# Performance work log

Measured on AMD Instinct MI355X. Metric: run time of the kernel, lower is better.

The kernel has to match this reference:

```python
import jax, jax.numpy as jnp
import numpy as np

DIM = 64
LEN = 256


def setup_inputs() -> dict:
    key = jax.random.key(0)
    ks = jax.random.split(key, 9)
    b, h, B = 4, 8, 16
    q = jax.random.normal(ks[0], (b, h, B, LEN, DIM), dtype=jnp.float32)
    k = jax.random.normal(ks[1], (b, h, B, LEN, DIM), dtype=jnp.float32)
    s = 1.0 / np.sqrt(DIM)
    Wq = jax.random.normal(ks[2], (1, DIM), dtype=jnp.float32) * s
    bq = jnp.ones((1,), dtype=jnp.float32)
    Wk = jax.random.normal(ks[3], (1, DIM), dtype=jnp.float32) * s
    bk = jnp.ones((1,), dtype=jnp.float32)
    sl = 1.0 / np.sqrt(LEN)
    W1 = jax.random.normal(ks[4], (1, LEN), dtype=jnp.float32) * sl
    W2a = jax.random.normal(ks[5], (LEN, LEN), dtype=jnp.float32) * sl
    W2b = jax.random.normal(ks[6], (1, LEN), dtype=jnp.float32) * sl
    return {"q": q, "k": k, "Wq": Wq, "bq": bq, "Wk": Wk, "bk": bk,
            "W1": W1, "W2a": W2a, "W2b": W2b}


def reference(q, k, Wq, bq, Wk, bk, W1, W2a, W2b):
    # Sigma_q/k: [b,h,B,L,1]
    Sigma_q = jnp.einsum('bhgid,od->bhgio', q, Wq) + bq
    Sigma_k = jnp.einsum('bhgjd,od->bhgjo', k, Wk) + bk
    # similarity: [b,h,B,L,L]
    sim = jnp.einsum('bhgid,bhgjd->bhgij', q, k)
    # outer product of the scalar projections: [b,h,B,L,L]
    Sigma = Sigma_q * jnp.swapaxes(Sigma_k, -1, -2)
    # zero the diagonal (sim - diag_embed(diag(sim)))
    eye = jnp.eye(sim.shape[-1], dtype=sim.dtype)
    sim_norm = sim * (1.0 - eye)
    # mlp1: Linear(L,1) over last axis -> [b,h,B,L]
    theta = jnp.einsum('bhgij,j->bhgi', sim_norm, W1[0])
    # mlp2: Linear(L,L) -> LeakyReLU(0.1) -> Linear(L,1) over axis i -> [b,h,B,1]
    hdn = jnp.einsum('bhgi,oi->bhgo', theta, W2a)
    hdn = jnp.where(hdn >= 0, hdn, 0.1 * hdn)
    theta = jnp.einsum('bhgi,oi->bhgo', hdn, W2b)[..., None]  # [b,h,B,1,1]
    sim = sim * Sigma
    attn = jax.nn.softmax(sim, axis=-1) * (sim > theta)
    return attn
```

## Files before the change

kernel.cpp:

```cpp
#include <hip/hip_runtime.h>
#include <math.h>

#define LL 256
#define DD 64

__launch_bounds__(512, 2)
__global__ void fused_attn_kernel(const float* __restrict__ q,
                                  const float* __restrict__ k,
                                  const float* __restrict__ Wq,
                                  const float* __restrict__ bq,
                                  const float* __restrict__ Wk,
                                  const float* __restrict__ bk,
                                  const float* __restrict__ W1,
                                  const float* __restrict__ W2a,
                                  const float* __restrict__ W2b,
                                  float* __restrict__ out)
{
    extern __shared__ float sm[];
    float* qT   = sm;
    float* kT   = sm + 64 * 256;
    float* sPq  = sm + 2 * 64 * 256;
    float* sPk  = sPq + 256;
    float* sPqk = sPk + 256;
    float* sTh  = sPqk + 256;
    float* sSq  = sTh + 256;
    float* sSk  = sSq + 256;
    float* kwred= sSk + 256;
    float* kw_s = kwred + 512;
    float* sRed = kw_s + 64;

    const int tid  = threadIdx.x;
    const int lane = tid & 63;
    const int wid  = tid >> 6;
    const int g    = blockIdx.x;
    const size_t gbase = (size_t)g * (LL * DD);
    const float4* q4 = (const float4*)(q + gbase);
    const float4* k4 = (const float4*)(k + gbase);

    const int dc = tid & 15;
    const float4 wq4 = ((const float4*)Wq)[dc];
    const float4 wk4 = ((const float4*)Wk)[dc];

    float kw0 = 0.f, kw1 = 0.f, kw2 = 0.f, kw3 = 0.f;

#pragma unroll
    for (int it = 0; it < 8; ++it) {
        const int f = it * 512 + tid;
        const int j = f >> 4;
        const float4 vq = q4[f];
        const float4 vk = k4[f];
        const int db = dc * 4;
        const int p  = db & 28;
        const int jx = j ^ p;
        qT[(db + 0) * 256 + jx] = vq.x;  kT[(db + 0) * 256 + jx] = vk.x;
        qT[(db + 1) * 256 + jx] = vq.y;  kT[(db + 1) * 256 + jx] = vk.y;
        qT[(db + 2) * 256 + jx] = vq.z;  kT[(db + 2) * 256 + jx] = vk.z;
        qT[(db + 3) * 256 + jx] = vq.w;  kT[(db + 3) * 256 + jx] = vk.w;

        const float w1j = W1[j];
        kw0 += w1j * vk.x; kw1 += w1j * vk.y; kw2 += w1j * vk.z; kw3 += w1j * vk.w;

        float pq  = vq.x * wq4.x + vq.y * wq4.y + vq.z * wq4.z + vq.w * wq4.w;
        float pk  = vk.x * wk4.x + vk.y * wk4.y + vk.z * wk4.z + vk.w * wk4.w;
        float pqk = vq.x * vk.x + vq.y * vk.y + vq.z * vk.z + vq.w * vk.w;
#pragma unroll
        for (int m = 1; m < 16; m <<= 1) {
            pq  += __shfl_xor(pq,  m);
            pk  += __shfl_xor(pk,  m);
            pqk += __shfl_xor(pqk, m);
        }
        if (dc == 0) { sPq[j] = pq; sPk[j] = pk; sPqk[j] = pqk; }
    }
    kw0 += __shfl_xor(kw0, 16); kw0 += __shfl_xor(kw0, 32);
    kw1 += __shfl_xor(kw1, 16); kw1 += __shfl_xor(kw1, 32);
    kw2 += __shfl_xor(kw2, 16); kw2 += __shfl_xor(kw2, 32);
    kw3 += __shfl_xor(kw3, 16); kw3 += __shfl_xor(kw3, 32);
    if (lane < 16) {
        float4 kv; kv.x = kw0; kv.y = kw1; kv.z = kw2; kv.w = kw3;
        ((float4*)kwred)[wid * 16 + lane] = kv;
    }
    __syncthreads();

    if (tid < 64) {
        float s = 0.f;
#pragma unroll
        for (int w = 0; w < 8; ++w) s += kwred[w * 64 + tid];
        kw_s[tid] = s;
    }
    __syncthreads();

    const float bq0 = bq[0], bk0 = bk[0];
    if (tid < 256) {
        const int i = tid;
        float qkw = 0.f;
#pragma unroll
        for (int d = 0; d < 64; ++d)
            qkw += qT[d * 256 + (i ^ (d & 28))] * kw_s[d];
        sTh[i] = qkw - W1[i] * sPqk[i];
        sSq[i] = sPq[i] + bq0;
        sSk[i] = sPk[i] + bk0;
    }
    __syncthreads();

    {
        const int o = tid >> 1, ih = tid & 1;
        const float4* wrow = (const float4*)W2a + o * 64 + ih * 32;
        const float4* th4  = (const float4*)sTh + ih * 32;
        float h = 0.f;
#pragma unroll 8
        for (int c = 0; c < 32; ++c) {
            const float4 wv = wrow[c];
            const float4 tv = th4[c];
            h += wv.x * tv.x + wv.y * tv.y + wv.z * tv.z + wv.w * tv.w;
        }
        h += __shfl_xor(h, 1);
        float contrib = 0.f;
        if (ih == 0) {
            const float hl = (h >= 0.f) ? h : 0.1f * h;
            contrib = hl * W2b[o];
        }
#pragma unroll
        for (int m = 1; m < 64; m <<= 1) contrib += __shfl_xor(contrib, m);
        if (lane == 0) sRed[wid] = contrib;
    }
    __syncthreads();

    const int rg = tid >> 4;
    const int cg = tid & 15;
    const int i0 = rg * 8;

    float acc[8][16];
#pragma unroll
    for (int r = 0; r < 8; ++r)
#pragma unroll
        for (int c = 0; c < 16; ++c) acc[r][c] = 0.f;

#pragma unroll 4
    for (int kk = 0; kk < 64; ++kk) {
        const float* qr = qT + kk * 256;
        const float* kr = kT + kk * 256;
        const int p = kk & 28;
        const float4 qa = *(const float4*)(qr + ((i0    ) ^ p));
        const float4 qb = *(const float4*)(qr + ((i0 + 4) ^ p));
        float4 kf[4];
        kf[0] = *(const float4*)(kr + ((cg * 4      ) ^ p));
        kf[1] = *(const float4*)(kr + ((cg * 4 +  64) ^ p));
        kf[2] = *(const float4*)(kr + ((cg * 4 + 128) ^ p));
        kf[3] = *(const float4*)(kr + ((cg * 4 + 192) ^ p));
        const float qv[8] = {qa.x, qa.y, qa.z, qa.w, qb.x, qb.y, qb.z, qb.w};
#pragma unroll
        for (int r = 0; r < 8; ++r) {
#pragma unroll
            for (int m = 0; m < 4; ++m) {
                acc[r][m * 4 + 0] += qv[r] * kf[m].x;
                acc[r][m * 4 + 1] += qv[r] * kf[m].y;
                acc[r][m * 4 + 2] += qv[r] * kf[m].z;
                acc[r][m * 4 + 3] += qv[r] * kf[m].w;
            }
        }
    }

    const float th_sc = sRed[0] + sRed[1] + sRed[2] + sRed[3] +
                        sRed[4] + sRed[5] + sRed[6] + sRed[7];
    float sq[8];
#pragma unroll
    for (int r = 0; r < 8; ++r) sq[r] = sSq[i0 + r];
    float sk[16];
#pragma unroll
    for (int m = 0; m < 4; ++m)
#pragma unroll
        for (int e = 0; e < 4; ++e) sk[m * 4 + e] = sSk[m * 64 + cg * 4 + e];

    float* og = out + (size_t)g * (LL * LL);

#pragma unroll
    for (int r = 0; r < 8; ++r) {
        float mx = -INFINITY;
#pragma unroll
        for (int c = 0; c < 16; ++c) {
            const float lg = acc[r][c] * sq[r] * sk[c];
            mx = fmaxf(mx, lg);
        }
        mx = fmaxf(mx, __shfl_xor(mx, 1));
        mx = fmaxf(mx, __shfl_xor(mx, 2));
        mx = fmaxf(mx, __shfl_xor(mx, 4));
        mx = fmaxf(mx, __shfl_xor(mx, 8));
        float sum = 0.f;
#pragma unroll
        for (int c = 0; c < 16; ++c) {
            const float lg = acc[r][c] * sq[r] * sk[c];
            const float pe = __expf(lg - mx);
            sum += pe;
            acc[r][c] = (lg > th_sc) ? pe : 0.f;
        }
        sum += __shfl_xor(sum, 1);
        sum += __shfl_xor(sum, 2);
        sum += __shfl_xor(sum, 4);
        sum += __shfl_xor(sum, 8);
        const float rinv = 1.0f / sum;
        const int row_off = (i0 + r) * 256 + cg * 4;
#pragma unroll
        for (int m = 0; m < 4; ++m) {
            float4 v;
            v.x = acc[r][m * 4 + 0] * rinv;
            v.y = acc[r][m * 4 + 1] * rinv;
            v.z = acc[r][m * 4 + 2] * rinv;
            v.w = acc[r][m * 4 + 3] * rinv;
            *(float4*)(og + row_off + m * 64) = v;
        }
    }
}

extern "C" void kernel_launch(void* const* d_in, const int* in_sizes, int n_in,
                              void* d_out, int out_size, void* d_ws, size_t ws_size,
                              hipStream_t stream) {
    const float* q   = (const float*)d_in[0];
    const float* k   = (const float*)d_in[1];
    const float* Wq  = (const float*)d_in[2];
    const float* bq  = (const float*)d_in[3];
    const float* Wk  = (const float*)d_in[4];
    const float* bk  = (const float*)d_in[5];
    const float* W1  = (const float*)d_in[6];
    const float* W2a = (const float*)d_in[7];
    const float* W2b = (const float*)d_in[8];
    float* out = (float*)d_out;

    const int ngroup = in_sizes[0] / (LL * DD);
    const size_t lds_bytes = (2 * 64 * 256 + 2120) * sizeof(float);

    (void)hipFuncSetAttribute((const void*)fused_attn_kernel,
                              hipFuncAttributeMaxDynamicSharedMemorySize,
                              (int)lds_bytes);

    fused_attn_kernel<<<dim3(ngroup), dim3(512), lds_bytes, stream>>>(
        q, k, Wq, bq, Wk, bk, W1, W2a, W2b, out);
}
```

Before: 253.4 us.

## Compute QK^T with bf16 MFMA using hi/lo split for fp32 accuracy

Replaces the scalar FP32 outer-product QK^T loop with MFMA 16x16x32 bf16 instructions. Q and K are each split into high and low bf16 parts, giving eight MFMAs per tile so the result stays close to fp32. K is stored in LDS as swizzled bf16 hi/lo rows, which halves LDS use, and Q fragments are loaded straight into registers. The theta projection and the softmax epilogue are rewritten to follow the MFMA output layout, at the cost of extra conversion work and uncoalesced scalar output stores.

```diff
diff --git a/kernel.cpp b/kernel.cpp
--- a/kernel.cpp
+++ b/kernel.cpp
@@ -4,22 +4,35 @@
 #define LL 256
 #define DD 64
 
+typedef __attribute__((ext_vector_type(8))) short bf16x8;
+typedef __attribute__((ext_vector_type(4))) float f32x4;
+
+static __device__ __forceinline__ unsigned short f2bf(float f) {
+    union { float f; unsigned u; } v; v.f = f;
+    unsigned r = v.u + 0x7fffu + ((v.u >> 16) & 1u);
+    return (unsigned short)(r >> 16);
+}
+static __device__ __forceinline__ float bf2f(unsigned short h) {
+    union { unsigned u; float f; } v; v.u = ((unsigned)h) << 16;
+    return v.f;
+}
+
 __launch_bounds__(512, 2)
-__global__ void fused_attn_kernel(const float* __restrict__ q,
-                                  const float* __restrict__ k,
-                                  const float* __restrict__ Wq,
-                                  const float* __restrict__ bq,
-                                  const float* __restrict__ Wk,
-                                  const float* __restrict__ bk,
-                                  const float* __restrict__ W1,
-                                  const float* __restrict__ W2a,
-                                  const float* __restrict__ W2b,
-                                  float* __restrict__ out)
+__global__ void fused_attn_mfma(const float* __restrict__ q,
+                                const float* __restrict__ k,
+                                const float* __restrict__ Wq,
+                                const float* __restrict__ bq,
+                                const float* __restrict__ Wk,
+                                const float* __restrict__ bk,
+                                const float* __restrict__ W1,
+                                const float* __restrict__ W2a,
+                                const float* __restrict__ W2b,
+                                float* __restrict__ out)
 {
-    extern __shared__ float sm[];
-    float* qT   = sm;
-    float* kT   = sm + 64 * 256;
-    float* sPq  = sm + 2 * 64 * 256;
+    extern __shared__ char smc[];
+    unsigned short* kHi = (unsigned short*)smc;
+    unsigned short* kLo = (unsigned short*)(smc + 32768);
+    float* sPq  = (float*)(smc + 65536);
     float* sPk  = sPq + 256;
     float* sPqk = sPk + 256;
     float* sTh  = sPqk + 256;
@@ -32,15 +45,28 @@
     const int tid  = threadIdx.x;
     const int lane = tid & 63;
     const int wid  = tid >> 6;
-    const int g    = blockIdx.x;
-    const size_t gbase = (size_t)g * (LL * DD);
-    const float4* q4 = (const float4*)(q + gbase);
+    const int r16  = lane & 15;
+    const int g4   = lane >> 4;
+    const int rbase = wid * 32;
+    const int gidx = blockIdx.x;
+    const size_t gbase = (size_t)gidx * (LL * DD);
+    const float* qg = q + gbase;
+    const float4* q4 = (const float4*)qg;
     const float4* k4 = (const float4*)(k + gbase);
+
+    float4 aq[2][2][2];
+#pragma unroll
+    for (int tr = 0; tr < 2; ++tr)
+#pragma unroll
+        for (int kk = 0; kk < 2; ++kk) {
+            const float* p = qg + (rbase + tr * 16 + r16) * DD + kk * 32 + g4 * 8;
+            aq[tr][kk][0] = ((const float4*)p)[0];
+            aq[tr][kk][1] = ((const float4*)p)[1];
+        }
 
     const int dc = tid & 15;
     const float4 wq4 = ((const float4*)Wq)[dc];
     const float4 wk4 = ((const float4*)Wk)[dc];
-
     float kw0 = 0.f, kw1 = 0.f, kw2 = 0.f, kw3 = 0.f;
 
 #pragma unroll
@@ -49,13 +75,20 @@
         const int j = f >> 4;
         const float4 vq = q4[f];
         const float4 vk = k4[f];
-        const int db = dc * 4;
-        const int p  = db & 28;
-        const int jx = j ^ p;
-        qT[(db + 0) * 256 + jx] = vq.x;  kT[(db + 0) * 256 + jx] = vk.x;
-        qT[(db + 1) * 256 + jx] = vq.y;  kT[(db + 1) * 256 + jx] = vk.y;
-        qT[(db + 2) * 256 + jx] = vq.z;  kT[(db + 2) * 256 + jx] = vk.z;
-        qT[(db + 3) * 256 + jx] = vq.w;  kT[(db + 3) * 256 + jx] = vk.w;
+
+        const int sw = (j & 7) << 4;
+        const int boff = j * 128 + ((dc * 8) ^ sw);
+        const unsigned short h0 = f2bf(vk.x), h1 = f2bf(vk.y),
+                             h2 = f2bf(vk.z), h3 = f2bf(vk.w);
+        uint2 hv, lv;
+        hv.x = (unsigned)h0 | ((unsigned)h1 << 16);
+        hv.y = (unsigned)h2 | ((unsigned)h3 << 16);
+        const unsigned short l0 = f2bf(vk.x - bf2f(h0)), l1 = f2bf(vk.y - bf2f(h1)),
+                             l2 = f2bf(vk.z - bf2f(h2)), l3 = f2bf(vk.w - bf2f(h3));
+        lv.x = (unsigned)l0 | ((unsigned)l1 << 16);
+        lv.y = (unsigned)l2 | ((unsigned)l3 << 16);
+        *(uint2*)((char*)kHi + boff) = hv;
+        *(uint2*)((char*)kLo + boff) = lv;
 
         const float w1j = W1[j];
         kw0 += w1j * vk.x; kw1 += w1j * vk.y; kw2 += w1j * vk.z; kw3 += w1j * vk.w;
@@ -79,8 +112,23 @@
         float4 kv; kv.x = kw0; kv.y = kw1; kv.z = kw2; kv.w = kw3;
         ((float4*)kwred)[wid * 16 + lane] = kv;
     }
-    __syncthreads();
-
+
+    bf16x8 qhi[2][2], qlo[2][2];
+#pragma unroll
+    for (int tr = 0; tr < 2; ++tr)
+#pragma unroll
+        for (int kk = 0; kk < 2; ++kk) {
+            const float fv[8] = {aq[tr][kk][0].x, aq[tr][kk][0].y, aq[tr][kk][0].z, aq[tr][kk][0].w,
+                                 aq[tr][kk][1].x, aq[tr][kk][1].y, aq[tr][kk][1].z, aq[tr][kk][1].w};
+#pragma unroll
+            for (int e = 0; e < 8; ++e) {
+                const unsigned short h = f2bf(fv[e]);
+                qhi[tr][kk][e] = (short)h;
+                qlo[tr][kk][e] = (short)f2bf(fv[e] - bf2f(h));
+            }
+        }
+
+    __syncthreads();
     if (tid < 64) {
         float s = 0.f;
 #pragma unroll
@@ -90,15 +138,27 @@
     __syncthreads();
 
     const float bq0 = bq[0], bk0 = bk[0];
-    if (tid < 256) {
-        const int i = tid;
-        float qkw = 0.f;
-#pragma unroll
-        for (int d = 0; d < 64; ++d)
-            qkw += qT[d * 256 + (i ^ (d & 28))] * kw_s[d];
-        sTh[i] = qkw - W1[i] * sPqk[i];
-        sSq[i] = sPq[i] + bq0;
-        sSk[i] = sPk[i] + bk0;
+#pragma unroll
+    for (int tr = 0; tr < 2; ++tr) {
+        const int row = rbase + tr * 16 + r16;
+        float s = 0.f;
+#pragma unroll
+        for (int kk = 0; kk < 2; ++kk) {
+            const int d0 = kk * 32 + g4 * 8;
+#pragma unroll
+            for (int e = 0; e < 8; ++e) {
+                const float qf = bf2f((unsigned short)qhi[tr][kk][e]) +
+                                 bf2f((unsigned short)qlo[tr][kk][e]);
+                s += qf * kw_s[d0 + e];
+            }
+        }
+        s += __shfl_xor(s, 16);
+        s += __shfl_xor(s, 32);
+        if (g4 == 0) {
+            sTh[row] = s - W1[row] * sPqk[row];
+            sSq[row] = sPq[row] + bq0;
+            sSk[row] = sPk[row] + bk0;
+        }
     }
     __syncthreads();
 
@@ -125,88 +185,77 @@
     }
     __syncthreads();
 
-    const int rg = tid >> 4;
-    const int cg = tid & 15;
-    const int i0 = rg * 8;
-
-    float acc[8][16];
-#pragma unroll
-    for (int r = 0; r < 8; ++r)
-#pragma unroll
-        for (int c = 0; c < 16; ++c) acc[r][c] = 0.f;
-
-#pragma unroll 4
-    for (int kk = 0; kk < 64; ++kk) {
-        const float* qr = qT + kk * 256;
-        const float* kr = kT + kk * 256;
-        const int p = kk & 28;
-        const float4 qa = *(const float4*)(qr + ((i0    ) ^ p));
-        const float4 qb = *(const float4*)(qr + ((i0 + 4) ^ p));
-        float4 kf[4];
-        kf[0] = *(const float4*)(kr + ((cg * 4      ) ^ p));
-        kf[1] = *(const float4*)(kr + ((cg * 4 +  64) ^ p));
-        kf[2] = *(const float4*)(kr + ((cg * 4 + 128) ^ p));
-        kf[3] = *(const float4*)(kr + ((cg * 4 + 192) ^ p));
-        const float qv[8] = {qa.x, qa.y, qa.z, qa.w, qb.x, qb.y, qb.z, qb.w};
-#pragma unroll
-        for (int r = 0; r < 8; ++r) {
-#pragma unroll
-            for (int m = 0; m < 4; ++m) {
-                acc[r][m * 4 + 0] += qv[r] * kf[m].x;
-                acc[r][m * 4 + 1] += qv[r] * kf[m].y;
-                acc[r][m * 4 + 2] += qv[r] * kf[m].z;
-                acc[r][m * 4 + 3] += qv[r] * kf[m].w;
-            }
+    f32x4 acc[2][16];
+#pragma unroll
+    for (int tr = 0; tr < 2; ++tr)
+#pragma unroll
+        for (int ct = 0; ct < 16; ++ct)
+            acc[tr][ct] = (f32x4){0.f, 0.f, 0.f, 0.f};
+
+#pragma unroll
+    for (int ct = 0; ct < 16; ++ct) {
+        const int rowk = ct * 16 + r16;
+        const int sw = (rowk & 7) << 4;
+        const char* ph = (const char*)kHi + rowk * 128;
+        const char* pl = (const char*)kLo + rowk * 128;
+        const bf16x8 bh0 = *(const bf16x8*)(ph + ((g4 * 16) ^ sw));
+        const bf16x8 bh1 = *(const bf16x8*)(ph + ((64 + g4 * 16) ^ sw));
+        const bf16x8 bl0 = *(const bf16x8*)(pl + ((g4 * 16) ^ sw));
+        const bf16x8 bl1 = *(const bf16x8*)(pl + ((64 + g4 * 16) ^ sw));
+#pragma unroll
+        for (int tr = 0; tr < 2; ++tr) {
+            f32x4 c = acc[tr][ct];
+            c = __builtin_amdgcn_mfma_f32_16x16x32_bf16(qhi[tr][0], bh0, c, 0, 0, 0);
+            c = __builtin_amdgcn_mfma_f32_16x16x32_bf16(qhi[tr][1], bh1, c, 0, 0, 0);
+            c = __builtin_amdgcn_mfma_f32_16x16x32_bf16(qhi[tr][0], bl0, c, 0, 0, 0);
+            c = __builtin_amdgcn_mfma_f32_16x16x32_bf16(qhi[tr][1], bl1, c, 0, 0, 0);
+            c = __builtin_amdgcn_mfma_f32_16x16x32_bf16(qlo[tr][0], bh0, c, 0, 0, 0);
+            c = __builtin_amdgcn_mfma_f32_16x16x32_bf16(qlo[tr][1], bh1, c, 0, 0, 0);
+            c = __builtin_amdgcn_mfma_f32_16x16x32_bf16(qlo[tr][0], bl0, c, 0, 0, 0);
+            c = __builtin_amdgcn_mfma_f32_16x16x32_bf16(qlo[tr][1], bl1, c, 0, 0, 0);
+            acc[tr][ct] = c;
         }
     }
 
     const float th_sc = sRed[0] + sRed[1] + sRed[2] + sRed[3] +
                         sRed[4] + sRed[5] + sRed[6] + sRed[7];
-    float sq[8];
-#pragma unroll
-    for (int r = 0; r < 8; ++r) sq[r] = sSq[i0 + r];
-    float sk[16];
-#pragma unroll
-    for (int m = 0; m < 4; ++m)
-#pragma unroll
-        for (int e = 0; e < 4; ++e) sk[m * 4 + e] = sSk[m * 64 + cg * 4 + e];
-
-    float* og = out + (size_t)g * (LL * LL);
-
-#pragma unroll
-    for (int r = 0; r < 8; ++r) {
-        float mx = -INFINITY;
-#pragma unroll
-        for (int c = 0; c < 16; ++c) {
-            const float lg = acc[r][c] * sq[r] * sk[c];
-            mx = fmaxf(mx, lg);
-        }
-        mx = fmaxf(mx, __shfl_xor(mx, 1));
-        mx = fmaxf(mx, __shfl_xor(mx, 2));
-        mx = fmaxf(mx, __shfl_xor(mx, 4));
-        mx = fmaxf(mx, __shfl_xor(mx, 8));
-        float sum = 0.f;
-#pragma unroll
-        for (int c = 0; c < 16; ++c) {
-            const float lg = acc[r][c] * sq[r] * sk[c];
-            const float pe = __expf(lg - mx);
-            sum += pe;
-            acc[r][c] = (lg > th_sc) ? pe : 0.f;
-        }
-        sum += __shfl_xor(sum, 1);
-        sum += __shfl_xor(sum, 2);
-        sum += __shfl_xor(sum, 4);
-        sum += __shfl_xor(sum, 8);
-        const float rinv = 1.0f / sum;
-        const int row_off = (i0 + r) * 256 + cg * 4;
-#pragma unroll
-        for (int m = 0; m < 4; ++m) {
-            float4 v;
-            v.x = acc[r][m * 4 + 0] * rinv;
-            v.y = acc[r][m * 4 + 1] * rinv;
-            v.z = acc[r][m * 4 + 2] * rinv;
-            v.w = acc[r][m * 4 + 3] * rinv;
-            *(float4*)(og + row_off + m * 64) = v;
+    float skv[16];
+#pragma unroll
+    for (int ct = 0; ct < 16; ++ct) skv[ct] = sSk[ct * 16 + r16];
+
+    float* og = out + (size_t)gidx * (LL * LL);
+#pragma unroll
+    for (int tr = 0; tr < 2; ++tr) {
+#pragma unroll
+        for (int r = 0; r < 4; ++r) {
+            const int row = rbase + tr * 16 + g4 * 4 + r;
+            const float sq = sSq[row];
+            float lg[16];
+            float mx = -INFINITY;
+#pragma unroll
+            for (int ct = 0; ct < 16; ++ct) {
+                lg[ct] = acc[tr][ct][r] * sq * skv[ct];
+                mx = fmaxf(mx, lg[ct]);
+            }
+            mx = fmaxf(mx, __shfl_xor(mx, 1));
+            mx = fmaxf(mx, __shfl_xor(mx, 2));
+            mx = fmaxf(mx, __shfl_xor(mx, 4));
+            mx = fmaxf(mx, __shfl_xor(mx, 8));
+            float sum = 0.f;
+#pragma unroll
+            for (int ct = 0; ct < 16; ++ct) {
+                const float pe = __expf(lg[ct] - mx);
+                sum += pe;
+                lg[ct] = (lg[ct] > th_sc) ? pe : 0.f;
+            }
+            sum += __shfl_xor(sum, 1);
+            sum += __shfl_xor(sum, 2);
+            sum += __shfl_xor(sum, 4);
+            sum += __shfl_xor(sum, 8);
+            const float rinv = 1.0f / sum;
+#pragma unroll
+            for (int ct = 0; ct < 16; ++ct)
+                og[row * LL + ct * 16 + r16] = lg[ct] * rinv;
         }
     }
 }
@@ -226,12 +275,12 @@
     float* out = (float*)d_out;
 
     const int ngroup = in_sizes[0] / (LL * DD);
-    const size_t lds_bytes = (2 * 64 * 256 + 2120) * sizeof(float);
-
-    (void)hipFuncSetAttribute((const void*)fused_attn_kernel,
+    const size_t lds_bytes = 65536 + 2120 * sizeof(float);
+
+    (void)hipFuncSetAttribute((const void*)fused_attn_mfma,
                               hipFuncAttributeMaxDynamicSharedMemorySize,
                               (int)lds_bytes);
 
-    fused_attn_kernel<<<dim3(ngroup), dim3(512), lds_bytes, stream>>>(
+    fused_attn_mfma<<<dim3(ngroup), dim3(512), lds_bytes, stream>>>(
         q, k, Wq, bq, Wk, bk, W1, W2a, W2b, out);
 }
```

Measured after the change: 227.0 us. 10.4% less time.
